# Optimization experiments

Hardware: AMD Instinct MI355X
Metric: run time of the kernel (lower is better)

The kernel has to match this reference:

```python
import jax, jax.numpy as jnp
import numpy as np

B, I, J, D_IN, D_INNER = 128, 1024, 1024, 256, 256


def setup_inputs() -> dict:
    key = jax.random.key(0)
    ks = jax.random.split(key, 6)
    std = 0.02
    return {
        "q": jax.random.normal(ks[0], (B, I, D_IN), dtype=jnp.float32),
        "k": jax.random.normal(ks[1], (B, J, D_IN), dtype=jnp.float32),
        "v": jax.random.normal(ks[2], (B, J, D_IN), dtype=jnp.float32),
        # torch nn.Linear weights: shape [out_features, in_features]
        "Wq": jax.random.normal(ks[3], (D_INNER, D_IN), dtype=jnp.float32) * std,
        "Wk": jax.random.normal(ks[4], (D_INNER, D_IN), dtype=jnp.float32) * std,
        "Wv": jax.random.normal(ks[5], (D_INNER, D_IN), dtype=jnp.float32) * std,
    }


def reference(q, k, v, Wq, Wk, Wv):
    # Linear projections (bias=False): x @ W.T
    qh = jnp.einsum('bid,ed->bie', q, Wq)  # [B, I, D_INNER]
    kh = jnp.einsum('bjd,ed->bje', k, Wk)  # [B, J, D_INNER]
    vh = jnp.einsum('bjd,ed->bje', v, Wv)  # [B, J, D_INNER] (embed_frame=True)
    scale = jnp.asarray(D_INNER, qh.dtype) ** -0.5  # heads == 1
    dots = jnp.einsum('bid,bjd->bij', qh, kh) * scale  # [B, I, J]
    attn = jax.nn.softmax(dots, axis=-1)
    out = jnp.einsum('bij,bjd->bid', attn, vh)  # [B, I, D_INNER]
    return out
```

## Files before the change

kernel.cpp:

```cpp
#include <hip/hip_runtime.h>
#include <stdint.h>


typedef __attribute__((ext_vector_type(4))) float f32x4;
typedef __attribute__((ext_vector_type(8))) short bf16x8;
typedef __attribute__((ext_vector_type(4))) uint32_t u32x4;
typedef __attribute__((ext_vector_type(4))) short s16x4;

#define MFMA(a, b, c) __builtin_amdgcn_mfma_f32_16x16x32_bf16(a, b, c, 0, 0, 0)

typedef const __attribute__((address_space(1))) uint32_t* gas1_t;
typedef __attribute__((address_space(3))) uint32_t* las3_t;

__device__ __forceinline__ void async16(const void* g, void* l) {
  __builtin_amdgcn_global_load_lds((gas1_t)g, (las3_t)l, 16, 0, 0);
}

__device__ __forceinline__ short f2bf_rne(float f) {
  uint32_t u = __builtin_bit_cast(uint32_t, f);
  u += 0x7FFFu + ((u >> 16) & 1u);
  return (short)(u >> 16);
}

__device__ __forceinline__ uint32_t pack2(float lo, float hi) {
  uint32_t a = __builtin_bit_cast(uint32_t, lo);
  uint32_t b = __builtin_bit_cast(uint32_t, hi);
  return (a >> 16) | (b & 0xFFFF0000u);
}

template <int N>
__device__ __forceinline__ void unit_wait() {
  __builtin_amdgcn_sched_barrier(0);
  if constexpr (N == 0)
    asm volatile("s_waitcnt vmcnt(0)" ::: "memory");
  else if constexpr (N == 1)
    asm volatile("s_waitcnt vmcnt(1)" ::: "memory");
  else
    asm volatile("s_waitcnt vmcnt(2)" ::: "memory");
  __builtin_amdgcn_s_barrier();
  __builtin_amdgcn_sched_barrier(0);
}

__global__ __launch_bounds__(256)
void wconv_kernel(const float* __restrict__ wq, const float* __restrict__ wk,
                  const float* __restrict__ wv, short* __restrict__ wbf) {
  const int mat = blockIdx.y;
  const float* w = (mat == 0) ? wq : (mat == 1) ? wk : wv;
  const int i = (blockIdx.x * 256 + threadIdx.x) * 4;
  f32x4 v = *(const f32x4*)(w + i);
  s16x4 o = {f2bf_rne(v.x), f2bf_rne(v.y), f2bf_rne(v.z), f2bf_rne(v.w)};
  *(s16x4*)(wbf + (size_t)mat * 65536 + i) = o;
}

__global__ __launch_bounds__(512)
void proj_kernel(const float* __restrict__ xq, const float* __restrict__ xk,
                 const float* __restrict__ xv, const short* __restrict__ wbf,
                 short* __restrict__ qh, short* __restrict__ kh,
                 short* __restrict__ vt) {
  __shared__ __align__(16) char smem[65536];
  short* ldst = (short*)smem;

  const int mat = blockIdx.y;
  const float* x = (mat == 0) ? xq : (mat == 1) ? xk : xv;
  const short* w = wbf + (size_t)mat * 65536;

  const int tile_m = blockIdx.x * 128;
  const int t = threadIdx.x;
  const int lane = t & 63, wid = t >> 6;
  const int wm = (wid & 1) * 64, wn = (wid >> 1) * 64;
  const int lr = lane & 15, lq = lane >> 4;

  f32x4 acc[4][4];
#pragma unroll
  for (int i = 0; i < 4; ++i)
#pragma unroll
    for (int j = 0; j < 4; ++j) acc[i][j] = (f32x4)0.0f;

  auto ISSUE = [&](int u) {
    if (u >= 16) return;
    char* base = smem + (u & 3) * 16384;
    const int k0 = (u >> 1) * 32;
    if ((u & 1) == 0) {
#pragma unroll
      for (int c = 0; c < 2; ++c) {
        int s = c * 512 + t;
        int rx = ((s >> 7) << 4) | (s & 15);
        int cx = (s >> 4) & 7;
        async16(x + (size_t)(tile_m + rx) * 256 + k0 + cx * 4, base + s * 16);
      }
    } else {
#pragma unroll
      for (int c = 0; c < 2; ++c) {
        int s = c * 512 + t;
        int rw = ((s >> 6) << 4) | (s & 15);
        int cw = (s >> 4) & 3;
        async16(w + (size_t)rw * 256 + k0 + cw * 8, base + s * 16);
      }
    }
  };

  ISSUE(0);
  ISSUE(1);
  for (int kk = 0; kk < 8; ++kk) {
    const int u = kk * 2 + 1;
    unit_wait<2>();
    ISSUE(u + 1);
    if (kk == 7) unit_wait<0>(); else unit_wait<2>();
    ISSUE(u + 2);
    const f32x4* x4 = (const f32x4*)(smem + ((u - 1) & 3) * 16384);
    const f32x4* w4 = (const f32x4*)(smem + (u & 3) * 16384);
    bf16x8 af[4], bf[4];
#pragma unroll
    for (int mi = 0; mi < 4; ++mi) {
      int row = wm + mi * 16 + lr;
      int sl = ((row >> 4) << 7) + (lq << 5) + (row & 15);
      f32x4 lo = x4[sl], hi = x4[sl + 16];
      u32x4 pk = {pack2(lo.x, lo.y), pack2(lo.z, lo.w), pack2(hi.x, hi.y),
                  pack2(hi.z, hi.w)};
      af[mi] = __builtin_bit_cast(bf16x8, pk);
    }
#pragma unroll
    for (int ni = 0; ni < 4; ++ni) {
      int col = wn + ni * 16 + lr;
      bf[ni] = __builtin_bit_cast(
          bf16x8, w4[((col >> 4) << 6) + (lq << 4) + (col & 15)]);
    }
    __builtin_amdgcn_s_setprio(1);
#pragma unroll
    for (int mi = 0; mi < 4; ++mi)
#pragma unroll
      for (int ni = 0; ni < 4; ++ni)
        acc[mi][ni] = MFMA(af[mi], bf[ni], acc[mi][ni]);
    __builtin_amdgcn_s_setprio(0);
  }
  __syncthreads();

  const float scale = (mat == 0) ? 0.0625f : 1.0f;
  const int bb = tile_m >> 10, j0 = tile_m & 1023;
#pragma unroll
  for (int p = 0; p < 2; ++p) {
    if (((wid >> 1) >> 1) == p) {
#pragma unroll
      for (int mi = 0; mi < 4; ++mi)
#pragma unroll
        for (int ni = 0; ni < 4; ++ni)
#pragma unroll
          for (int r = 0; r < 4; ++r) {
            int m = wm + mi * 16 + lq * 4 + r;
            int n = ((wid >> 1) & 1) * 64 + ni * 16 + lr;
            short bv = f2bf_rne(acc[mi][ni][r] * scale);
            if (mat < 2) ldst[m * 136 + n] = bv;
            else         ldst[n * 136 + m] = bv;
          }
    }
    __syncthreads();
#pragma unroll
    for (int q = 0; q < 4; ++q) {
      int idx = q * 512 + t;
      int row = idx >> 4;
      int col8 = (idx & 15) * 8;
      bf16x8 vdat = *(const bf16x8*)(ldst + row * 136 + col8);
      short* dst;
      if (mat < 2) {
        short* o = (mat == 0) ? qh : kh;
        dst = o + (size_t)(tile_m + row) * 256 + p * 128 + col8;
      } else {
        dst = vt + ((size_t)(bb * 256 + p * 128 + row)) * 1024 + j0 + col8;
      }
      *(bf16x8*)dst = vdat;
    }
    __syncthreads();
  }
}

__global__ __launch_bounds__(512)
void attn_kernel(const short* __restrict__ qh, const short* __restrict__ kh,
                 const short* __restrict__ vt, float* __restrict__ out) {
  __shared__ __align__(16) char smem[32768 + 34816];
  short* ldsS = (short*)smem;
  short* ldsP = (short*)(smem + 32768);

  const int b = blockIdx.x;
  const int i0 = blockIdx.y * 128;
  const int t = threadIdx.x;
  const int lane = t & 63, wid = t >> 6;
  const int rg = wid >> 1, cg = wid & 1;
  const int lr = lane & 15, lq = lane >> 4;
  const size_t bq = (size_t)b * 262144;

  f32x4 oacc[2][8];
#pragma unroll
  for (int i = 0; i < 2; ++i)
#pragma unroll
    for (int j = 0; j < 8; ++j) oacc[i][j] = (f32x4)0.0f;
  float lsum[8];
#pragma unroll
  for (int i = 0; i < 8; ++i) lsum[i] = 0.0f;

  auto ISSUE = [&](int u) {
    if (u >= 192) return;
    short* base = ldsS + (u & 3) * 4096;
    const int jt = u / 24, r = u % 24;
    const int j0 = jt * 128;
    const int s = t;
    if (r < 16) {
      const int k0 = (r >> 1) * 32;
      int rr = ((s >> 6) << 4) | (s & 15);
      int c8 = (s >> 4) & 3;
      if ((r & 1) == 0)
        async16(qh + bq + (size_t)(i0 + rr) * 256 + k0 + c8 * 8, base + s * 8);
      else
        async16(kh + bq + (size_t)(j0 + rr) * 256 + k0 + c8 * 8, base + s * 8);
    } else {
      const int v = r - 16;
      const int kc = v >> 1, half = v & 1;
      int d = (half << 7) | ((s >> 6) << 4) | (s & 15);
      int c8 = (s >> 4) & 3;
      async16(vt + bq + (size_t)d * 1024 + j0 + kc * 32 + c8 * 8, base + s * 8);
    }
  };

  ISSUE(0);
  ISSUE(1);
  int u = 0;

  for (int jt = 0; jt < 8; ++jt) {
    f32x4 sacc[2][4];
#pragma unroll
    for (int i = 0; i < 2; ++i)
#pragma unroll
      for (int j = 0; j < 4; ++j) sacc[i][j] = (f32x4)0.0f;

    for (int kk = 0; kk < 8; ++kk) {
      unit_wait<1>();
      ISSUE(u + 2);
      ++u;
      unit_wait<1>();
      ISSUE(u + 2);
      const f32x4* q4 = (const f32x4*)(ldsS + ((u - 1) & 3) * 4096);
      const f32x4* k4 = (const f32x4*)(ldsS + (u & 3) * 4096);
      bf16x8 aq[2], bk[4];
#pragma unroll
      for (int mi = 0; mi < 2; ++mi) {
        int row = rg * 32 + mi * 16 + lr;
        aq[mi] = __builtin_bit_cast(
            bf16x8, q4[((row >> 4) << 6) + (lq << 4) + (row & 15)]);
      }
#pragma unroll
      for (int ni = 0; ni < 4; ++ni) {
        int col = cg * 64 + ni * 16 + lr;
        bk[ni] = __builtin_bit_cast(
            bf16x8, k4[((col >> 4) << 6) + (lq << 4) + (col & 15)]);
      }
      __builtin_amdgcn_s_setprio(1);
#pragma unroll
      for (int mi = 0; mi < 2; ++mi)
#pragma unroll
        for (int ni = 0; ni < 4; ++ni)
          sacc[mi][ni] = MFMA(aq[mi], bk[ni], sacc[mi][ni]);
      __builtin_amdgcn_s_setprio(0);
      ++u;
    }

    float prt[8];
#pragma unroll
    for (int i = 0; i < 8; ++i) prt[i] = 0.0f;
#pragma unroll
    for (int mi = 0; mi < 2; ++mi)
#pragma unroll
      for (int ni = 0; ni < 4; ++ni)
#pragma unroll
        for (int r = 0; r < 4; ++r) {
          float e = __expf(sacc[mi][ni][r]);
          prt[mi * 4 + r] += e;
          int m = rg * 32 + mi * 16 + lq * 4 + r;
          int jc = cg * 64 + ni * 16 + lr;
          ldsP[m * 136 + jc] = f2bf_rne(e);
        }
#pragma unroll
    for (int v = 0; v < 8; ++v) {
      float p = prt[v];
      p += __shfl_xor(p, 1, 64);
      p += __shfl_xor(p, 2, 64);
      p += __shfl_xor(p, 4, 64);
      p += __shfl_xor(p, 8, 64);
      lsum[v] += p;
    }
    asm volatile("s_waitcnt lgkmcnt(0)" ::: "memory");

    for (int kc = 0; kc < 4; ++kc) {
      unit_wait<1>();
      ISSUE(u + 2);
      ++u;
      if (jt == 7 && kc == 3) unit_wait<0>(); else unit_wait<1>();
      ISSUE(u + 2);
      const f32x4* v4 =
          (const f32x4*)(ldsS + ((cg ? u : (u - 1)) & 3) * 4096);
      const f32x4* p4 = (const f32x4*)ldsP;
      bf16x8 pf[2], vf[8];
#pragma unroll
      for (int mi = 0; mi < 2; ++mi) {
        int m = rg * 32 + mi * 16 + lr;
        pf[mi] = __builtin_bit_cast(bf16x8, p4[m * 17 + kc * 4 + lq]);
      }
#pragma unroll
      for (int ni = 0; ni < 8; ++ni) {
        vf[ni] = __builtin_bit_cast(bf16x8, v4[ni * 64 + (lq << 4) + lr]);
      }
      __builtin_amdgcn_s_setprio(1);
#pragma unroll
      for (int mi = 0; mi < 2; ++mi)
#pragma unroll
        for (int ni = 0; ni < 8; ++ni)
          oacc[mi][ni] = MFMA(pf[mi], vf[ni], oacc[mi][ni]);
      __builtin_amdgcn_s_setprio(0);
      ++u;
    }
  }
  __syncthreads();

  float* lscr = (float*)ldsP;
  if (lr == 0) {
#pragma unroll
    for (int mi = 0; mi < 2; ++mi)
#pragma unroll
      for (int r = 0; r < 4; ++r)
        lscr[wid * 32 + mi * 16 + lq * 4 + r] = lsum[mi * 4 + r];
  }
  __syncthreads();
  float inv[8];
#pragma unroll
  for (int mi = 0; mi < 2; ++mi)
#pragma unroll
    for (int r = 0; r < 4; ++r) {
      float tot = lsum[mi * 4 + r] + lscr[(wid ^ 1) * 32 + mi * 16 + lq * 4 + r];
      inv[mi * 4 + r] = 1.0f / tot;
    }
#pragma unroll
  for (int mi = 0; mi < 2; ++mi)
#pragma unroll
    for (int ni = 0; ni < 8; ++ni)
#pragma unroll
      for (int r = 0; r < 4; ++r) {
        int i = i0 + rg * 32 + mi * 16 + lq * 4 + r;
        int d = cg * 128 + ni * 16 + lr;
        out[bq + (size_t)i * 256 + d] = oacc[mi][ni][r] * inv[mi * 4 + r];
      }
}

extern "C" void kernel_launch(void* const* d_in, const int* in_sizes, int n_in,
                              void* d_out, int out_size, void* d_ws,
                              size_t ws_size, hipStream_t stream) {
  (void)in_sizes; (void)n_in; (void)out_size; (void)ws_size;
  const float* q  = (const float*)d_in[0];
  const float* k  = (const float*)d_in[1];
  const float* v  = (const float*)d_in[2];
  const float* wq = (const float*)d_in[3];
  const float* wk = (const float*)d_in[4];
  const float* wv = (const float*)d_in[5];
  float* out = (float*)d_out;

  short* qh = (short*)d_ws;
  short* kh = qh + (size_t)33554432;
  short* vt = kh + (size_t)33554432;
  short* wbf = (short*)d_out;

  wconv_kernel<<<dim3(64, 3), dim3(256), 0, stream>>>(wq, wk, wv, wbf);
  proj_kernel<<<dim3(1024, 3), dim3(512), 0, stream>>>(
      q, k, v, wbf, qh, kh, vt);
  attn_kernel<<<dim3(128, 8), dim3(512), 0, stream>>>(qh, kh, vt, out);
}
```

Measured before the change: 738.6 us.

## Keep Q tile in registers and deepen K/V async prefetch pipeline

Each wave now loads its Q fragments once from global memory into registers (16 bf16x8 per lane) instead of re-streaming the Q tile through LDS for every one of the 8 key tiles. This removes a quarter of the async global-to-LDS traffic and the LDS reads for Q. With the freed slots, the prefetch distance grows from 2 to 3 units over the 4-buffer ring, and the inner loops are unrolled. The cost is higher register pressure at 512 threads per block, and a ring this deep leaves little slack against buffer reuse hazards.

```diff
diff --git a/kernel.cpp b/kernel.cpp
--- a/kernel.cpp
+++ b/kernel.cpp
@@ -188,6 +188,17 @@
   const int lr = lane & 15, lq = lane >> 4;
   const size_t bq = (size_t)b * 262144;
 
+  bf16x8 qreg[2][8];
+  {
+    const short* qb = qh + bq + (size_t)(i0 + rg * 32 + lr) * 256 + lq * 8;
+#pragma unroll
+    for (int mi = 0; mi < 2; ++mi)
+#pragma unroll
+      for (int kk = 0; kk < 8; ++kk)
+        qreg[mi][kk] =
+            *(const bf16x8*)(qb + (size_t)(mi * 16) * 256 + kk * 32);
+  }
+
   f32x4 oacc[2][8];
 #pragma unroll
   for (int i = 0; i < 2; ++i)
@@ -198,21 +209,18 @@
   for (int i = 0; i < 8; ++i) lsum[i] = 0.0f;
 
   auto ISSUE = [&](int u) {
-    if (u >= 192) return;
+    if (u >= 128) return;
     short* base = ldsS + (u & 3) * 4096;
-    const int jt = u / 24, r = u % 24;
+    const int jt = u >> 4, r = u & 15;
     const int j0 = jt * 128;
     const int s = t;
-    if (r < 16) {
-      const int k0 = (r >> 1) * 32;
+    if (r < 8) {
+      const int k0 = r * 32;
       int rr = ((s >> 6) << 4) | (s & 15);
       int c8 = (s >> 4) & 3;
-      if ((r & 1) == 0)
-        async16(qh + bq + (size_t)(i0 + rr) * 256 + k0 + c8 * 8, base + s * 8);
-      else
-        async16(kh + bq + (size_t)(j0 + rr) * 256 + k0 + c8 * 8, base + s * 8);
+      async16(kh + bq + (size_t)(j0 + rr) * 256 + k0 + c8 * 8, base + s * 8);
     } else {
-      const int v = r - 16;
+      const int v = r - 8;
       const int kc = v >> 1, half = v & 1;
       int d = (half << 7) | ((s >> 6) << 4) | (s & 15);
       int c8 = (s >> 4) & 3;
@@ -222,6 +230,7 @@
 
   ISSUE(0);
   ISSUE(1);
+  ISSUE(2);
   int u = 0;
 
   for (int jt = 0; jt < 8; ++jt) {
@@ -231,21 +240,12 @@
 #pragma unroll
       for (int j = 0; j < 4; ++j) sacc[i][j] = (f32x4)0.0f;
 
+#pragma unroll
     for (int kk = 0; kk < 8; ++kk) {
-      unit_wait<1>();
-      ISSUE(u + 2);
-      ++u;
-      unit_wait<1>();
-      ISSUE(u + 2);
-      const f32x4* q4 = (const f32x4*)(ldsS + ((u - 1) & 3) * 4096);
+      unit_wait<2>();
+      ISSUE(u + 3);
       const f32x4* k4 = (const f32x4*)(ldsS + (u & 3) * 4096);
-      bf16x8 aq[2], bk[4];
-#pragma unroll
-      for (int mi = 0; mi < 2; ++mi) {
-        int row = rg * 32 + mi * 16 + lr;
-        aq[mi] = __builtin_bit_cast(
-            bf16x8, q4[((row >> 4) << 6) + (lq << 4) + (row & 15)]);
-      }
+      bf16x8 bk[4];
 #pragma unroll
       for (int ni = 0; ni < 4; ++ni) {
         int col = cg * 64 + ni * 16 + lr;
@@ -257,7 +257,7 @@
       for (int mi = 0; mi < 2; ++mi)
 #pragma unroll
         for (int ni = 0; ni < 4; ++ni)
-          sacc[mi][ni] = MFMA(aq[mi], bk[ni], sacc[mi][ni]);
+          sacc[mi][ni] = MFMA(qreg[mi][kk], bk[ni], sacc[mi][ni]);
       __builtin_amdgcn_s_setprio(0);
       ++u;
     }
@@ -288,15 +288,16 @@
     }
     asm volatile("s_waitcnt lgkmcnt(0)" ::: "memory");
 
+    const f32x4* p4 = (const f32x4*)ldsP;
+#pragma unroll
     for (int kc = 0; kc < 4; ++kc) {
-      unit_wait<1>();
-      ISSUE(u + 2);
+      if (jt == 7 && kc == 3) unit_wait<1>(); else unit_wait<2>();
+      ISSUE(u + 3);
       ++u;
-      if (jt == 7 && kc == 3) unit_wait<0>(); else unit_wait<1>();
-      ISSUE(u + 2);
+      if (jt == 7 && kc == 3) unit_wait<0>(); else unit_wait<2>();
+      ISSUE(u + 3);
       const f32x4* v4 =
           (const f32x4*)(ldsS + ((cg ? u : (u - 1)) & 3) * 4096);
-      const f32x4* p4 = (const f32x4*)ldsP;
       bf16x8 pf[2], vf[8];
 #pragma unroll
       for (int mi = 0; mi < 2; ++mi) {
```

Measured after the change: 670.3 us. 9.3% less time.
